# Kernel optimization log

Hardware: AMD Instinct MI355X
Metric: run time of the kernel (lower is better)

The kernel has to match this reference:

```python
import jax, jax.numpy as jnp
import numpy as np

DIM = 1024
NUM_HEADS = 16
HEAD_DIM = DIM // NUM_HEADS
SCALING = HEAD_DIM ** (-0.5)


def setup_inputs() -> dict:
    key = jax.random.key(0)
    ks = jax.random.split(key, 9)
    B, S = 2, 2048
    s = DIM ** -0.5  # ~ torch Linear init scale
    inp = {
        "x": jax.random.normal(ks[0], (B, S, DIM), dtype=jnp.float32),
        "wq": jax.random.uniform(ks[1], (DIM, DIM), jnp.float32, -s, s),
        "bq": jax.random.uniform(ks[2], (DIM,), jnp.float32, -s, s),
        "wk": jax.random.uniform(ks[3], (DIM, DIM), jnp.float32, -s, s),
        "bk": jax.random.uniform(ks[4], (DIM,), jnp.float32, -s, s),
        "wv": jax.random.uniform(ks[5], (DIM, DIM), jnp.float32, -s, s),
        "bv": jax.random.uniform(ks[6], (DIM,), jnp.float32, -s, s),
        "wo": jax.random.uniform(ks[7], (DIM, DIM), jnp.float32, -s, s),
        "bo": jax.random.uniform(ks[8], (DIM,), jnp.float32, -s, s),
    }
    return inp


def reference(x, wq, bq, wk, bk, wv, bv, wo, bo):
    B, S, D = x.shape
    # projections (weights stored [out,in] like torch Linear -> x @ W.T + b)
    q = (x @ wq.T + bq).reshape(B, S, NUM_HEADS, HEAD_DIM)
    k = (x @ wk.T + bk).reshape(B, S, NUM_HEADS, HEAD_DIM)
    v = (x @ wv.T + bv).reshape(B, S, NUM_HEADS, HEAD_DIM)
    # [B,H,S,S] scores, scaled
    scores = jnp.einsum("bqhd,bkhd->bhqk", q, k) * SCALING
    attn = jax.nn.softmax(scores, axis=-1)
    # dropout p=0.0 (eval): identity
    out = jnp.einsum("bhqk,bkhd->bqhd", attn, v).reshape(B, S, D)
    return out @ wo.T + bo
```

## Files before the change

kernel.cpp:

```cpp
#include <hip/hip_runtime.h>

#define DIM 1024
#define NHEADS 16
#define HDIM 64
#define BATCH 2
#define SEQ 2048
#define MTOT (BATCH*SEQ)
#define QSCALE 0.18033688011112042f
#define XN ((size_t)MTOT*DIM)
#define WN ((size_t)DIM*DIM)

typedef __attribute__((ext_vector_type(8))) short short8;
typedef __attribute__((ext_vector_type(4))) float f32x4;
typedef __attribute__((ext_vector_type(16))) float f32x16;
typedef __attribute__((ext_vector_type(2))) int int2v;

static __device__ __forceinline__ unsigned short bf16rne(float f) {
    unsigned u = __builtin_bit_cast(unsigned, f);
    return (unsigned short)((u + 0x7fffu + ((u >> 16) & 1u)) >> 16);
}

static __device__ __forceinline__ void gld16(const void* g, void* l) {
    __builtin_amdgcn_global_load_lds((const __attribute__((address_space(1))) void*)g,
                                     (__attribute__((address_space(3))) void*)l, 16, 0, 0);
}

static __device__ __forceinline__ f32x16 mfma32(short8 a, short8 b, f32x16 c) {
    return __builtin_amdgcn_mfma_f32_32x32x16_bf16(a, b, c, 0, 0, 0);
}

__global__ __launch_bounds__(256)
void prep(const float* __restrict__ x, const float* __restrict__ wq, const float* __restrict__ wk,
          const float* __restrict__ wv, const float* __restrict__ wo, unsigned short* __restrict__ dst)
{
    const size_t i = ((size_t)blockIdx.x*256 + threadIdx.x)*8;
    const float* s; size_t o;
    if (i < XN)           { s = x;  o = i; }
    else if (i < XN+WN)   { s = wq; o = i - XN; }
    else if (i < XN+2*WN) { s = wk; o = i - XN - WN; }
    else if (i < XN+3*WN) { s = wv; o = i - XN - 2*WN; }
    else                  { s = wo; o = i - XN - 3*WN; }
    float4 a = *(const float4*)(s + o);
    float4 b = *(const float4*)(s + o + 4);
    uint4 w;
    w.x = (unsigned)bf16rne(a.x) | ((unsigned)bf16rne(a.y) << 16);
    w.y = (unsigned)bf16rne(a.z) | ((unsigned)bf16rne(a.w) << 16);
    w.z = (unsigned)bf16rne(b.x) | ((unsigned)bf16rne(b.y) << 16);
    w.w = (unsigned)bf16rne(b.z) | ((unsigned)bf16rne(b.w) << 16);
    *(uint4*)&dst[i] = w;
}

__global__ __launch_bounds__(256)
void gemm_qkv(const unsigned short* __restrict__ A,
              const unsigned short* __restrict__ W0, const unsigned short* __restrict__ W1,
              const unsigned short* __restrict__ W2,
              const float* __restrict__ b0, const float* __restrict__ b1, const float* __restrict__ b2,
              unsigned short* __restrict__ o0, unsigned short* __restrict__ o1, unsigned short* __restrict__ o2)
{
    __shared__ __align__(16) unsigned short As[3][4096];
    __shared__ __align__(16) unsigned short Bs[3][4096];
    const int t = threadIdx.x, wid = t >> 6, lane = t & 63;
    const int lr = lane & 15, lg = lane >> 4;
    const int bid = blockIdx.y * 24 + blockIdx.x;
    const int swz = (bid & 7) * 96 + (bid >> 3);
    const int sx = swz % 24, sy = swz / 24;
    const int widx = sx >> 3;
    const int n0 = (sx & 7) << 7;
    const int m0 = sy << 7;
    const unsigned short* W = widx == 0 ? W0 : (widx == 1 ? W1 : W2);
    const float* bias        = widx == 0 ? b0 : (widx == 1 ? b1 : b2);
    const float scale        = widx == 0 ? QSCALE : 1.0f;
    unsigned short* out      = widx == 0 ? o0 : (widx == 1 ? o1 : o2);

    const int wm = wid >> 1, wn = wid & 1;
    const int f0 = 2*wid, f1 = f0 + 1;
    const unsigned short* Ag0 = A + (size_t)(m0 + f0*16 + lr)*DIM + lg*8;
    const unsigned short* Ag1 = A + (size_t)(m0 + f1*16 + lr)*DIM + lg*8;
    const unsigned short* Bg0 = W + (size_t)(n0 + f0*16 + lr)*DIM + lg*8;
    const unsigned short* Bg1 = W + (size_t)(n0 + f1*16 + lr)*DIM + lg*8;

    auto stage = [&](int tt, int slot) {
        const int ko = tt * 32;
        gld16(Ag0 + ko, &As[slot][f0*512]); gld16(Ag1 + ko, &As[slot][f1*512]);
        gld16(Bg0 + ko, &Bs[slot][f0*512]); gld16(Bg1 + ko, &Bs[slot][f1*512]);
    };

    f32x4 acc[4][4] = {};
    stage(0, 0); stage(1, 1);
    int c0 = 0, c1 = 1, c2 = 2;

    for (int it = 0; it < DIM/32; ++it) {
        if (it < DIM/32 - 2) { asm volatile("s_waitcnt vmcnt(4)" ::: "memory"); }
        else                 { asm volatile("s_waitcnt vmcnt(0)" ::: "memory"); }
        __builtin_amdgcn_s_barrier();
        short8 af[4], bf[4];
        #pragma unroll
        for (int i = 0; i < 4; ++i) af[i] = *(const short8*)&As[c0][(wm*4+i)*512 + lane*8];
        #pragma unroll
        for (int i = 0; i < 4; ++i) bf[i] = *(const short8*)&Bs[c0][(wn*4+i)*512 + lane*8];
        if (it + 2 < DIM/32) stage(it + 2, c2);
        __builtin_amdgcn_s_setprio(1);
        #pragma unroll
        for (int mb = 0; mb < 4; ++mb)
            #pragma unroll
            for (int nb = 0; nb < 4; ++nb)
                acc[mb][nb] = __builtin_amdgcn_mfma_f32_16x16x32_bf16(af[mb], bf[nb], acc[mb][nb], 0, 0, 0);
        __builtin_amdgcn_s_setprio(0);
        const int tmp = c0; c0 = c1; c1 = c2; c2 = tmp;
    }

    #pragma unroll
    for (int nb = 0; nb < 4; ++nb) {
        const int col = n0 + wn*64 + nb*16 + lr;
        const float bv = bias[col];
        #pragma unroll
        for (int mb = 0; mb < 4; ++mb) {
            #pragma unroll
            for (int j = 0; j < 4; ++j) {
                const int row = m0 + wm*64 + mb*16 + lg*4 + j;
                out[(size_t)row*DIM + col] = bf16rne((acc[mb][nb][j] + bv) * scale);
            }
        }
    }
}

__global__ __launch_bounds__(256)
void gemm_o(const unsigned short* __restrict__ A, const unsigned short* __restrict__ W,
            const float* __restrict__ bias, float* __restrict__ fo)
{
    __shared__ __align__(16) unsigned short As[3][2048];
    __shared__ __align__(16) unsigned short Bs[3][4096];
    const int t = threadIdx.x, wid = t >> 6, lane = t & 63;
    const int lr = lane & 15, lg = lane >> 4;
    const int bid = blockIdx.y * 8 + blockIdx.x;
    const int swz = (bid & 7) * 64 + (bid >> 3);
    const int n0 = (swz & 7) << 7;
    const int m0 = (swz >> 3) << 6;
    const int wm = wid >> 1, wn = wid & 1;

    const int fa = wid;
    const int g0 = 2*wid, g1 = g0 + 1;
    const unsigned short* Ag  = A + (size_t)(m0 + fa*16 + lr)*DIM + lg*8;
    const unsigned short* Bg0 = W + (size_t)(n0 + g0*16 + lr)*DIM + lg*8;
    const unsigned short* Bg1 = W + (size_t)(n0 + g1*16 + lr)*DIM + lg*8;

    auto stage = [&](int tt, int slot) {
        const int ko = tt * 32;
        gld16(Ag + ko, &As[slot][fa*512]);
        gld16(Bg0 + ko, &Bs[slot][g0*512]); gld16(Bg1 + ko, &Bs[slot][g1*512]);
    };

    f32x4 acc[2][4] = {};
    stage(0, 0); stage(1, 1);
    int c0 = 0, c1 = 1, c2 = 2;

    for (int it = 0; it < DIM/32; ++it) {
        if (it < DIM/32 - 2) { asm volatile("s_waitcnt vmcnt(3)" ::: "memory"); }
        else                 { asm volatile("s_waitcnt vmcnt(0)" ::: "memory"); }
        __builtin_amdgcn_s_barrier();
        short8 af[2], bf[4];
        #pragma unroll
        for (int i = 0; i < 2; ++i) af[i] = *(const short8*)&As[c0][(wm*2+i)*512 + lane*8];
        #pragma unroll
        for (int i = 0; i < 4; ++i) bf[i] = *(const short8*)&Bs[c0][(wn*4+i)*512 + lane*8];
        if (it + 2 < DIM/32) stage(it + 2, c2);
        __builtin_amdgcn_s_setprio(1);
        #pragma unroll
        for (int mb = 0; mb < 2; ++mb)
            #pragma unroll
            for (int nb = 0; nb < 4; ++nb)
                acc[mb][nb] = __builtin_amdgcn_mfma_f32_16x16x32_bf16(af[mb], bf[nb], acc[mb][nb], 0, 0, 0);
        __builtin_amdgcn_s_setprio(0);
        const int tmp = c0; c0 = c1; c1 = c2; c2 = tmp;
    }

    #pragma unroll
    for (int nb = 0; nb < 4; ++nb) {
        const int col = n0 + wn*64 + nb*16 + lr;
        const float bv = bias[col];
        #pragma unroll
        for (int mb = 0; mb < 2; ++mb) {
            #pragma unroll
            for (int j = 0; j < 4; ++j) {
                const int row = m0 + wm*32 + mb*16 + lg*4 + j;
                fo[(size_t)row*DIM + col] = acc[mb][nb][j] + bv;
            }
        }
    }
}

__global__ __launch_bounds__(256)
void transpose_v(const unsigned short* __restrict__ V, unsigned short* __restrict__ Vt)
{
    __shared__ unsigned short tile[64][66];
    const int t  = threadIdx.x;
    const int st = blockIdx.x;
    const int bh = blockIdx.y;
    const int b = bh >> 4, h = bh & 15;
    const int sr = t >> 3;
    const int dc = (t & 7) * 8;

    #pragma unroll
    for (int r = 0; r < 2; ++r) {
        const int s = r*32 + sr;
        short8 v = *(const short8*)(V + (size_t)(b*SEQ + st*64 + s)*DIM + h*HDIM + dc);
        #pragma unroll
        for (int e = 0; e < 8; ++e) tile[s][dc + e] = (unsigned short)v[e];
    }
    __syncthreads();
    #pragma unroll
    for (int r = 0; r < 2; ++r) {
        const int d = r*32 + sr;
        short8 ov;
        #pragma unroll
        for (int e = 0; e < 8; ++e) ov[e] = (short)tile[dc + e][d];
        *(short8*)(Vt + (size_t)bh*HDIM*SEQ + (size_t)d*SEQ + st*64 + dc) = ov;
    }
}

struct PA { short8 p[4]; };

static __device__ __forceinline__ PA softmax_pack(const f32x16& s0, const f32x16& s1, float& lsum) {
    float rsum = 0.f;
    unsigned pw0[4][2], pw1[4][2];
    #pragma unroll
    for (int r1 = 0; r1 < 4; ++r1)
        #pragma unroll
        for (int tt = 0; tt < 2; ++tt) {
            float pa_ = __builtin_amdgcn_exp2f(s0[4*r1+2*tt]);
            float pb_ = __builtin_amdgcn_exp2f(s0[4*r1+2*tt+1]);
            float pc_ = __builtin_amdgcn_exp2f(s1[4*r1+2*tt]);
            float pd_ = __builtin_amdgcn_exp2f(s1[4*r1+2*tt+1]);
            rsum += (pa_ + pb_) + (pc_ + pd_);
            asm("v_cvt_pk_bf16_f32 %0, %1, %2" : "=v"(pw0[r1][tt]) : "v"(pa_), "v"(pb_));
            asm("v_cvt_pk_bf16_f32 %0, %1, %2" : "=v"(pw1[r1][tt]) : "v"(pc_), "v"(pd_));
        }
    rsum += __shfl_xor(rsum, 32);
    lsum += rsum;
    PA r;
    #pragma unroll
    for (int ss = 0; ss < 4; ++ss) {
        union { short8 s8; unsigned u[4]; } pu;
        #pragma unroll
        for (int tt = 0; tt < 2; ++tt) {
            const unsigned a = (ss >> 1) ? pw1[2*(ss&1)][tt]   : pw0[2*(ss&1)][tt];
            const unsigned b = (ss >> 1) ? pw1[2*(ss&1)+1][tt] : pw0[2*(ss&1)+1][tt];
            int2v sw = __builtin_amdgcn_permlane32_swap((int)a, (int)b, false, false);
            pu.u[tt]     = (unsigned)sw[0];
            pu.u[2 + tt] = (unsigned)sw[1];
        }
        r.p[ss] = pu.s8;
    }
    return r;
}

__global__ __launch_bounds__(256)
void attn_mfma2(const unsigned short* __restrict__ Q, const unsigned short* __restrict__ Kg,
                const unsigned short* __restrict__ Vt, unsigned short* __restrict__ O)
{
    __shared__ __align__(16) unsigned short Ks[4][4096];
    __shared__ __align__(16) unsigned short Vs[4][4096];
    const int t = threadIdx.x, wid = t >> 6, lane = t & 63;
    const int l31 = lane & 31, h = lane >> 5;
    const int bid = blockIdx.y * 16 + blockIdx.x;
    const int swz = (bid & 7) * 64 + (bid >> 3);
    const int qt = swz & 15, bh = swz >> 4;
    const int b = bh >> 4, hh = bh & 15;
    const size_t qkbase = (size_t)b*SEQ*DIM + (size_t)hh*HDIM;
    const unsigned short* Qb = Q + qkbase;
    const unsigned short* Kb = Kg + qkbase;
    const unsigned short* Vb = Vt + (size_t)bh*HDIM*SEQ;
    unsigned short*       Ob = O + qkbase;
    const int q0 = qt*128 + wid*32;

    short8 qf[4];
    #pragma unroll
    for (int ds = 0; ds < 4; ++ds)
        qf[ds] = *(const short8*)&Qb[(size_t)(q0 + l31)*DIM + ds*16 + h*8];

    const int f0 = 2*wid, f1 = f0 + 1;
    const unsigned short* Kg0 = &Kb[(size_t)((f0>>2)*32 + l31)*DIM + (f0&3)*16 + h*8];
    const unsigned short* Kg1 = &Kb[(size_t)((f1>>2)*32 + l31)*DIM + (f1&3)*16 + h*8];
    const unsigned short* Vg0 = &Vb[(size_t)((f0>>2)*32 + l31)*SEQ + (f0&3)*16 + h*8];
    const unsigned short* Vg1 = &Vb[(size_t)((f1>>2)*32 + l31)*SEQ + (f1&3)*16 + h*8];

    auto stage = [&](int tn) {
        const size_t koK = (size_t)tn * 64 * DIM;
        const size_t koV = (size_t)tn * 64;
        const int bb = tn & 3;
        gld16(Kg0 + koK, &Ks[bb][f0*512]); gld16(Kg1 + koK, &Ks[bb][f1*512]);
        gld16(Vg0 + koV, &Vs[bb][f0*512]); gld16(Vg1 + koV, &Vs[bb][f1*512]);
    };

    f32x16 ctx0 = {}, ctx1 = {};
    float lsum = 0.0f;

    stage(0); stage(1);

    const int NW = SEQ/128;
    for (int w = 0; w < NW; ++w) {
        const int t0 = 2*w;
        const int ba = t0 & 3, bb2 = (t0+1) & 3;
        const bool more = (w + 1 < NW);

        if (more) { asm volatile("s_waitcnt vmcnt(4)" ::: "memory"); }
        else      { asm volatile("s_waitcnt vmcnt(0)" ::: "memory"); }
        __builtin_amdgcn_s_barrier();
        if (more) stage(t0 + 2);

        f32x16 s0a = {}, s1a = {};
        __builtin_amdgcn_s_setprio(1);
        #pragma unroll
        for (int ds = 0; ds < 4; ++ds) {
            short8 kf0 = *(const short8*)&Ks[ba][ds*512 + lane*8];
            short8 kf1 = *(const short8*)&Ks[ba][(4+ds)*512 + lane*8];
            s0a = mfma32(kf0, qf[ds], s0a);
            s1a = mfma32(kf1, qf[ds], s1a);
        }
        __builtin_amdgcn_s_setprio(0);

        PA pa = softmax_pack(s0a, s1a, lsum);

        if (more) { asm volatile("s_waitcnt vmcnt(4)" ::: "memory"); }
        else      { asm volatile("s_waitcnt vmcnt(0)" ::: "memory"); }
        __builtin_amdgcn_s_barrier();
        if (more) stage(t0 + 3);

        f32x16 s0b = {}, s1b = {};
        __builtin_amdgcn_s_setprio(1);
        #pragma unroll
        for (int ds = 0; ds < 4; ++ds) {
            short8 kf0 = *(const short8*)&Ks[bb2][ds*512 + lane*8];
            short8 kf1 = *(const short8*)&Ks[bb2][(4+ds)*512 + lane*8];
            s0b = mfma32(kf0, qf[ds], s0b);
            s1b = mfma32(kf1, qf[ds], s1b);
        }
        #pragma unroll
        for (int ss = 0; ss < 4; ++ss) {
            short8 vf0 = *(const short8*)&Vs[ba][ss*512 + lane*8];
            short8 vf1 = *(const short8*)&Vs[ba][(4+ss)*512 + lane*8];
            ctx0 = mfma32(pa.p[ss], vf0, ctx0);
            ctx1 = mfma32(pa.p[ss], vf1, ctx1);
        }
        __builtin_amdgcn_s_setprio(0);

        PA pb = softmax_pack(s0b, s1b, lsum);

        __builtin_amdgcn_s_setprio(1);
        #pragma unroll
        for (int ss = 0; ss < 4; ++ss) {
            short8 vf0 = *(const short8*)&Vs[bb2][ss*512 + lane*8];
            short8 vf1 = *(const short8*)&Vs[bb2][(4+ss)*512 + lane*8];
            ctx0 = mfma32(pb.p[ss], vf0, ctx0);
            ctx1 = mfma32(pb.p[ss], vf1, ctx1);
        }
        __builtin_amdgcn_s_setprio(0);
    }

    const float linv = 1.0f / lsum;
    #pragma unroll
    for (int r = 0; r < 16; ++r) {
        const int qrow = (r&3) + 8*(r>>2) + 4*h;
        const float nm = __shfl(linv, qrow);
        unsigned short* p = &Ob[(size_t)(q0 + qrow)*DIM + l31];
        p[0]  = bf16rne(ctx0[r] * nm);
        p[32] = bf16rne(ctx1[r] * nm);
    }
}

extern "C" void kernel_launch(void* const* d_in, const int* in_sizes, int n_in,
                              void* d_out, int out_size, void* d_ws, size_t ws_size,
                              hipStream_t stream) {
    const float* x  = (const float*)d_in[0];
    const float* wq = (const float*)d_in[1];
    const float* bq = (const float*)d_in[2];
    const float* wk = (const float*)d_in[3];
    const float* bk = (const float*)d_in[4];
    const float* wv = (const float*)d_in[5];
    const float* bv = (const float*)d_in[6];
    const float* wo = (const float*)d_in[7];
    const float* bo = (const float*)d_in[8];
    float* out = (float*)d_out;

    unsigned short* Xb  = (unsigned short*)d_ws;
    unsigned short* Wqb = Xb  + XN;
    unsigned short* Wkb = Wqb + WN;
    unsigned short* Wvb = Wkb + WN;
    unsigned short* Wob = Wvb + WN;
    unsigned short* Qb  = Wob + WN;
    unsigned short* Kb  = Qb  + XN;
    unsigned short* Vb  = Kb  + XN;
    unsigned short* Vtb = Vb  + XN;
    unsigned short* Cb  = Xb;

    prep<<<4096, 256, 0, stream>>>(x, wq, wk, wv, wo, Xb);

    gemm_qkv<<<dim3(24, 32), 256, 0, stream>>>(Xb, Wqb, Wkb, Wvb, bq, bk, bv, Qb, Kb, Vb);

    transpose_v<<<dim3(SEQ/64, BATCH*NHEADS), 256, 0, stream>>>(Vb, Vtb);
    attn_mfma2<<<dim3(SEQ/128, BATCH*NHEADS), 256, 0, stream>>>(Qb, Kb, Vtb, Cb);

    gemm_o<<<dim3(8, 64), 256, 0, stream>>>(Cb, Wob, bo, out);
}
```

Baseline: 141.9 us.

## Write K and V in attention-tile-packed layout for contiguous tile loads

The QKV GEMM epilogue now writes K straight into a per-(batch,head) tile-packed layout that matches the MFMA fragment order the attention kernel stages into LDS. The V transpose kernel likewise emits V in the same packed tile layout. The attention kernel then loads each 64-key tile as one contiguous 8KB block instead of strided rows with a DIM or SEQ stride. This should improve global load coalescing in attention, but the K epilogue stores become scattered 2-byte writes.

```diff
diff --git a/kernel.cpp b/kernel.cpp
--- a/kernel.cpp
+++ b/kernel.cpp
@@ -109,16 +109,38 @@
         const int tmp = c0; c0 = c1; c1 = c2; c2 = tmp;
     }
 
-    #pragma unroll
-    for (int nb = 0; nb < 4; ++nb) {
-        const int col = n0 + wn*64 + nb*16 + lr;
-        const float bv = bias[col];
-        #pragma unroll
-        for (int mb = 0; mb < 4; ++mb) {
+    if (widx == 1) {
+        #pragma unroll
+        for (int nb = 0; nb < 4; ++nb) {
+            const int col = n0 + wn*64 + nb*16 + lr;
+            const int hh = col >> 6, dd = col & 63;
+            const float bv = bias[col];
+            const int fr_d = dd >> 4, ln_d = ((dd >> 3) & 1) << 5, e = dd & 7;
             #pragma unroll
-            for (int j = 0; j < 4; ++j) {
-                const int row = m0 + wm*64 + mb*16 + lg*4 + j;
-                out[(size_t)row*DIM + col] = bf16rne((acc[mb][nb][j] + bv) * scale);
+            for (int mb = 0; mb < 4; ++mb) {
+                #pragma unroll
+                for (int j = 0; j < 4; ++j) {
+                    const int row = m0 + wm*64 + mb*16 + lg*4 + j;
+                    const int bb = row >> 11, s_in = row & (SEQ-1);
+                    const int kt = s_in >> 6, s_t = s_in & 63;
+                    const size_t off = ((size_t)((bb*NHEADS + hh)*32 + kt))*4096
+                                     + ((s_t >> 5)*4 + fr_d)*512 + ((s_t & 31) | ln_d)*8 + e;
+                    out[off] = bf16rne(acc[mb][nb][j] + bv);
+                }
+            }
+        }
+    } else {
+        #pragma unroll
+        for (int nb = 0; nb < 4; ++nb) {
+            const int col = n0 + wn*64 + nb*16 + lr;
+            const float bv = bias[col];
+            #pragma unroll
+            for (int mb = 0; mb < 4; ++mb) {
+                #pragma unroll
+                for (int j = 0; j < 4; ++j) {
+                    const int row = m0 + wm*64 + mb*16 + lg*4 + j;
+                    out[(size_t)row*DIM + col] = bf16rne((acc[mb][nb][j] + bv) * scale);
+                }
             }
         }
     }
@@ -190,7 +212,7 @@
 }
 
 __global__ __launch_bounds__(256)
-void transpose_v(const unsigned short* __restrict__ V, unsigned short* __restrict__ Vt)
+void pack_v(const unsigned short* __restrict__ V, unsigned short* __restrict__ Vp)
 {
     __shared__ unsigned short tile[64][66];
     const int t  = threadIdx.x;
@@ -208,13 +230,17 @@
         for (int e = 0; e < 8; ++e) tile[s][dc + e] = (unsigned short)v[e];
     }
     __syncthreads();
+    unsigned short* outb = Vp + ((size_t)bh*32 + st)*4096;
     #pragma unroll
     for (int r = 0; r < 2; ++r) {
-        const int d = r*32 + sr;
+        const int idx = t + r*256;
+        const int fr = idx >> 6, ln = idx & 63;
+        const int s0 = (fr & 3)*16 + (ln >> 5)*8;
+        const int d  = (fr >> 2)*32 + (ln & 31);
         short8 ov;
         #pragma unroll
-        for (int e = 0; e < 8; ++e) ov[e] = (short)tile[dc + e][d];
-        *(short8*)(Vt + (size_t)bh*HDIM*SEQ + (size_t)d*SEQ + st*64 + dc) = ov;
+        for (int e = 0; e < 8; ++e) ov[e] = (short)tile[s0 + e][d];
+        *(short8*)(outb + fr*512 + ln*8) = ov;
     }
 }
 
@@ -255,8 +281,8 @@
 }
 
 __global__ __launch_bounds__(256)
-void attn_mfma2(const unsigned short* __restrict__ Q, const unsigned short* __restrict__ Kg,
-                const unsigned short* __restrict__ Vt, unsigned short* __restrict__ O)
+void attn_mfma2(const unsigned short* __restrict__ Q, const unsigned short* __restrict__ Kp,
+                const unsigned short* __restrict__ Vp, unsigned short* __restrict__ O)
 {
     __shared__ __align__(16) unsigned short Ks[4][4096];
     __shared__ __align__(16) unsigned short Vs[4][4096];
@@ -268,8 +294,6 @@
     const int b = bh >> 4, hh = bh & 15;
     const size_t qkbase = (size_t)b*SEQ*DIM + (size_t)hh*HDIM;
     const unsigned short* Qb = Q + qkbase;
-    const unsigned short* Kb = Kg + qkbase;
-    const unsigned short* Vb = Vt + (size_t)bh*HDIM*SEQ;
     unsigned short*       Ob = O + qkbase;
     const int q0 = qt*128 + wid*32;
 
@@ -279,17 +303,16 @@
         qf[ds] = *(const short8*)&Qb[(size_t)(q0 + l31)*DIM + ds*16 + h*8];
 
     const int f0 = 2*wid, f1 = f0 + 1;
-    const unsigned short* Kg0 = &Kb[(size_t)((f0>>2)*32 + l31)*DIM + (f0&3)*16 + h*8];
-    const unsigned short* Kg1 = &Kb[(size_t)((f1>>2)*32 + l31)*DIM + (f1&3)*16 + h*8];
-    const unsigned short* Vg0 = &Vb[(size_t)((f0>>2)*32 + l31)*SEQ + (f0&3)*16 + h*8];
-    const unsigned short* Vg1 = &Vb[(size_t)((f1>>2)*32 + l31)*SEQ + (f1&3)*16 + h*8];
+    const unsigned short* Kg0 = Kp + (size_t)bh*32*4096 + f0*512 + lane*8;
+    const unsigned short* Kg1 = Kg0 + 512;
+    const unsigned short* Vg0 = Vp + (size_t)bh*32*4096 + f0*512 + lane*8;
+    const unsigned short* Vg1 = Vg0 + 512;
 
     auto stage = [&](int tn) {
-        const size_t koK = (size_t)tn * 64 * DIM;
-        const size_t koV = (size_t)tn * 64;
+        const size_t ko = (size_t)tn * 4096;
         const int bb = tn & 3;
-        gld16(Kg0 + koK, &Ks[bb][f0*512]); gld16(Kg1 + koK, &Ks[bb][f1*512]);
-        gld16(Vg0 + koV, &Vs[bb][f0*512]); gld16(Vg1 + koV, &Vs[bb][f1*512]);
+        gld16(Kg0 + ko, &Ks[bb][f0*512]); gld16(Kg1 + ko, &Ks[bb][f1*512]);
+        gld16(Vg0 + ko, &Vs[bb][f0*512]); gld16(Vg1 + ko, &Vs[bb][f1*512]);
     };
 
     f32x16 ctx0 = {}, ctx1 = {};
@@ -388,17 +411,17 @@
     unsigned short* Wvb = Wkb + WN;
     unsigned short* Wob = Wvb + WN;
     unsigned short* Qb  = Wob + WN;
-    unsigned short* Kb  = Qb  + XN;
-    unsigned short* Vb  = Kb  + XN;
-    unsigned short* Vtb = Vb  + XN;
+    unsigned short* Kpb = Qb  + XN;
+    unsigned short* Vb  = Kpb + XN;
+    unsigned short* Vpb = Vb  + XN;
     unsigned short* Cb  = Xb;
 
     prep<<<4096, 256, 0, stream>>>(x, wq, wk, wv, wo, Xb);
 
-    gemm_qkv<<<dim3(24, 32), 256, 0, stream>>>(Xb, Wqb, Wkb, Wvb, bq, bk, bv, Qb, Kb, Vb);
-
-    transpose_v<<<dim3(SEQ/64, BATCH*NHEADS), 256, 0, stream>>>(Vb, Vtb);
-    attn_mfma2<<<dim3(SEQ/128, BATCH*NHEADS), 256, 0, stream>>>(Qb, Kb, Vtb, Cb);
+    gemm_qkv<<<dim3(24, 32), 256, 0, stream>>>(Xb, Wqb, Wkb, Wvb, bq, bk, bv, Qb, Kpb, Vb);
+
+    pack_v<<<dim3(SEQ/64, BATCH*NHEADS), 256, 0, stream>>>(Vb, Vpb);
+    attn_mfma2<<<dim3(SEQ/128, BATCH*NHEADS), 256, 0, stream>>>(Qb, Kpb, Vpb, Cb);
 
     gemm_o<<<dim3(8, 64), 256, 0, stream>>>(Cb, Wob, bo, out);
 }
```

Measured after the change: 151.8 us. 7.0% more time.
